# Kernel optimization log

Measured on AMD Instinct MI355X. Metric: run time of the kernel, lower is better.

## Reference

```python
import jax, jax.numpy as jnp
import numpy as np


def _prelu(x, p):
    # PReLU with a single learnable slope (torch default num_parameters=1)
    return jnp.where(x >= 0, x, p[0] * x)


def setup_inputs() -> dict:
    key = jax.random.key(0)
    ks = jax.random.split(key, 8)
    B, R, N, S, Din, Dout = 8, 4, 2048, 6, 32, 32
    return {
        "theta_param": jax.random.uniform(ks[0], (R, S), dtype=jnp.float32),
        "t_param": jax.random.uniform(ks[1], (R, S), dtype=jnp.float32),
        "a_input_batched": jax.random.uniform(ks[2], (B, R, N, N), dtype=jnp.float32),
        "x_input_batched": jax.random.normal(ks[3], (B, R, N, Din), dtype=jnp.float32),
        "fc_w": jax.random.normal(ks[4], (R, Din, Dout), dtype=jnp.float32) * 0.05,
        "fc_b": jax.random.normal(ks[5], (R, Dout), dtype=jnp.float32) * 0.05,
        "conv_w": jax.random.normal(ks[6], (R, R), dtype=jnp.float32) * 0.05,
        "conv_b": jax.random.normal(ks[7], (R,), dtype=jnp.float32) * 0.05,
        "prelu0": jnp.full((1,), 0.25, dtype=jnp.float32),
        "prelu1": jnp.full((1,), 0.25, dtype=jnp.float32),
    }


def reference(theta_param, t_param, a_input_batched, x_input_batched,
              fc_w, fc_b, conv_w, conv_b, prelu0, prelu1):
    # The inner diffusion-step loop is sum_s theta[r,s]*t[r,s] -> scalar per relation.
    coef = jnp.sum(theta_param * t_param, axis=1)              # [R]
    # diffusion_mat = coef[r] * A[b,r]; fold the scalar into the matmul result.
    diff_feat = jnp.einsum('brnm,brmd->brnd', a_input_batched, x_input_batched)
    diff_feat = coef[None, :, None, None] * diff_feat          # [B,R,N,Din]
    # Per-relation linear layer.
    fc_out = jnp.einsum('brnd,rde->brne', diff_feat, fc_w) + fc_b[None, :, None, :]
    h = _prelu(fc_out, prelu0)                                 # activation0
    # 1x1 Conv2d over the relation channel == [R,R] mixing matrix + bias.
    mixed = jnp.einsum('brne,qr->bqne', h, conv_w) + conv_b[None, :, None, None]
    latent = _prelu(mixed, prelu1)                             # activation1
    return latent  # original returns (latent, latent) — same tensor twice
```

## Files before the change

kernel.cpp:

```cpp
#include <hip/hip_runtime.h>
#include <hip/hip_bf16.h>

typedef __attribute__((ext_vector_type(8))) short  bf16x8;
typedef __attribute__((ext_vector_type(4))) float  f32x4;
typedef __attribute__((ext_vector_type(4))) int    i32x4;

#define B_   8
#define R_   4
#define N_   2048
#define S_   6
#define DIN  32
#define DOUT 32

__global__ __launch_bounds__(256) void prep_xw(
    const float* __restrict__ theta, const float* __restrict__ tpar,
    const float* __restrict__ X,     const float* __restrict__ fcw,
    __hip_bfloat16* __restrict__ xwt)
{
    int br    = blockIdx.x >> 5;
    int mtile = blockIdx.x & 31;
    int r     = br & 3;
    int t     = threadIdx.x;
    int m     = mtile * 64 + (t & 63);
    int egrp  = t >> 6;

    float coef = 0.f;
#pragma unroll
    for (int s = 0; s < S_; ++s) coef += theta[r * S_ + s] * tpar[r * S_ + s];

    const float* xrow = X + ((size_t)br * N_ + m) * DIN;
    float xr[DIN];
#pragma unroll
    for (int i = 0; i < DIN / 4; ++i) {
        f32x4 v = *(const f32x4*)(xrow + i * 4);
        xr[i * 4 + 0] = v.x; xr[i * 4 + 1] = v.y;
        xr[i * 4 + 2] = v.z; xr[i * 4 + 3] = v.w;
    }
#pragma unroll
    for (int eb = 0; eb < 8; ++eb) {
        int e = egrp * 8 + eb;
        float acc = 0.f;
#pragma unroll
        for (int d = 0; d < DIN; ++d) acc += xr[d] * fcw[(r * DIN + d) * DOUT + e];
        xwt[((size_t)br * DOUT + e) * N_ + m] = __float2bfloat16(coef * acc);
    }
}

__global__ __launch_bounds__(256) void fused_main(
    const float* __restrict__ A,   const __hip_bfloat16* __restrict__ xwt,
    const float* __restrict__ fcb, const float* __restrict__ cw,
    const float* __restrict__ cb,  const float* __restrict__ p0p,
    const float* __restrict__ p1p, float* __restrict__ out)
{
    __shared__ float hlds[R_][16][DOUT + 1];

    int b    = blockIdx.x >> 7;
    int tile = blockIdx.x & 127;
    int n0   = tile * 16;
    int t    = threadIdx.x;
    int r    = t >> 6;
    int l    = t & 63;
    int row16 = l & 15;
    int kg    = l >> 4;

    const float*  Ap  = A + (((size_t)(b * R_ + r)) * N_ + (n0 + row16)) * N_ + kg * 8;
    const ushort* xw  = (const ushort*)xwt + ((size_t)(b * R_ + r) * DOUT) * N_;
    const ushort* xw0 = xw + (size_t)row16 * N_        + kg * 8;
    const ushort* xw1 = xw + (size_t)(16 + row16) * N_ + kg * 8;

    f32x4 acc0 = {0.f, 0.f, 0.f, 0.f};
    f32x4 acc1 = {0.f, 0.f, 0.f, 0.f};

#pragma unroll 4
    for (int kt = 0; kt < N_ / 32; ++kt) {
        f32x4 a0 = *(const f32x4*)(Ap + kt * 32);
        f32x4 a1 = *(const f32x4*)(Ap + kt * 32 + 4);
        i32x4 bv0 = *(const i32x4*)(xw0 + kt * 32);
        i32x4 bv1 = *(const i32x4*)(xw1 + kt * 32);
        i32x4 av;
        asm("v_cvt_pk_bf16_f32 %0, %1, %2" : "=v"(av.x) : "v"(a0.x), "v"(a0.y));
        asm("v_cvt_pk_bf16_f32 %0, %1, %2" : "=v"(av.y) : "v"(a0.z), "v"(a0.w));
        asm("v_cvt_pk_bf16_f32 %0, %1, %2" : "=v"(av.z) : "v"(a1.x), "v"(a1.y));
        asm("v_cvt_pk_bf16_f32 %0, %1, %2" : "=v"(av.w) : "v"(a1.z), "v"(a1.w));
        bf16x8 af = __builtin_bit_cast(bf16x8, av);
        bf16x8 b0 = __builtin_bit_cast(bf16x8, bv0);
        bf16x8 b1 = __builtin_bit_cast(bf16x8, bv1);
        acc0 = __builtin_amdgcn_mfma_f32_16x16x32_bf16(af, b0, acc0, 0, 0, 0);
        acc1 = __builtin_amdgcn_mfma_f32_16x16x32_bf16(af, b1, acc1, 0, 0, 0);
    }

    float p0 = p0p[0], p1 = p1p[0];

#pragma unroll
    for (int j = 0; j < 4; ++j) {
        int rw = kg * 4 + j;
        float v0 = acc0[j] + fcb[r * DOUT + row16];
        float v1 = acc1[j] + fcb[r * DOUT + 16 + row16];
        hlds[r][rw][row16]      = v0 >= 0.f ? v0 : p0 * v0;
        hlds[r][rw][16 + row16] = v1 >= 0.f ? v1 : p0 * v1;
    }
    __syncthreads();

    int q = r;
    float c0 = cw[q * R_ + 0], c1 = cw[q * R_ + 1];
    float c2 = cw[q * R_ + 2], c3 = cw[q * R_ + 3];
    float cbq = cb[q];
    int e  = l & 31;
    int rg = l >> 5;
#pragma unroll
    for (int i = 0; i < 8; ++i) {
        int row = rg * 8 + i;
        float mx = cbq + c0 * hlds[0][row][e] + c1 * hlds[1][row][e]
                       + c2 * hlds[2][row][e] + c3 * hlds[3][row][e];
        float lat = mx >= 0.f ? mx : p1 * mx;
        out[(((size_t)b * R_ + q) * N_ + (n0 + row)) * DOUT + e] = lat;
    }
}

extern "C" void kernel_launch(void* const* d_in, const int* in_sizes, int n_in,
                              void* d_out, int out_size, void* d_ws, size_t ws_size,
                              hipStream_t stream)
{
    const float* theta = (const float*)d_in[0];
    const float* tpar  = (const float*)d_in[1];
    const float* A     = (const float*)d_in[2];
    const float* X     = (const float*)d_in[3];
    const float* fcw   = (const float*)d_in[4];
    const float* fcb   = (const float*)d_in[5];
    const float* cw    = (const float*)d_in[6];
    const float* cb    = (const float*)d_in[7];
    const float* p0    = (const float*)d_in[8];
    const float* p1    = (const float*)d_in[9];

    __hip_bfloat16* xwt = (__hip_bfloat16*)d_ws;

    prep_xw<<<B_ * R_ * (N_ / 64), 256, 0, stream>>>(theta, tpar, X, fcw, xwt);
    fused_main<<<B_ * (N_ / 16), 256, 0, stream>>>(A, xwt, fcb, cw, cb, p0, p1,
                                                   (float*)d_out);
}
```

Baseline: 154.9 us.

## Double-buffer A tiles in LDS via async global_load_lds with swizzled layout

Replaces the direct per-thread global loads of the fp32 adjacency rows with asynchronous global-to-LDS copies into a double-buffered, XOR-swizzled shared tile. Each iteration now covers 64 columns (two MFMAs per accumulator), and B operands are prefetched one step ahead with explicit vmcnt waits. The goal is to overlap the dominant A streaming with compute and hide memory latency. It adds 32KB of LDS per block, which may reduce occupancy, and relies on hand-placed waitcnts without workgroup barriers between waves, which works only because each wave owns its own LDS region.

Result: faster. 140.6 us (-9.2%).

```diff
diff --git a/kernel.cpp b/kernel.cpp
--- a/kernel.cpp
+++ b/kernel.cpp
@@ -4,6 +4,8 @@
 typedef __attribute__((ext_vector_type(8))) short  bf16x8;
 typedef __attribute__((ext_vector_type(4))) float  f32x4;
 typedef __attribute__((ext_vector_type(4))) int    i32x4;
+typedef __attribute__((address_space(3))) void       as3void;
+typedef const __attribute__((address_space(1))) void as1void;
 
 #define B_   8
 #define R_   4
@@ -11,6 +13,7 @@
 #define S_   6
 #define DIN  32
 #define DOUT 32
+#define NT   32
 
 __global__ __launch_bounds__(256) void prep_xw(
     const float* __restrict__ theta, const float* __restrict__ tpar,
@@ -52,7 +55,7 @@
     const float* __restrict__ cb,  const float* __restrict__ p0p,
     const float* __restrict__ p1p, float* __restrict__ out)
 {
-    __shared__ float hlds[R_][16][DOUT + 1];
+    __shared__ char smem[32768];
 
     int b    = blockIdx.x >> 7;
     int tile = blockIdx.x & 127;
@@ -62,35 +65,94 @@
     int l    = t & 63;
     int row16 = l & 15;
     int kg    = l >> 4;
-
-    const float*  Ap  = A + (((size_t)(b * R_ + r)) * N_ + (n0 + row16)) * N_ + kg * 8;
-    const ushort* xw  = (const ushort*)xwt + ((size_t)(b * R_ + r) * DOUT) * N_;
-    const ushort* xw0 = xw + (size_t)row16 * N_        + kg * 8;
-    const ushort* xw1 = xw + (size_t)(16 + row16) * N_ + kg * 8;
+    int swzr  = (row16 & 7) << 4;
+    int ldsbase = r * 4096;
+
+    const char* Ab = (const char*)(A + (((size_t)(b * R_ + r)) * N_ + n0) * N_);
+    const char* srcp[4];
+#pragma unroll
+    for (int i = 0; i < 4; ++i) {
+        int row = i * 4 + kg;
+        srcp[i] = Ab + (size_t)row * (N_ * 4) + (((l & 15) * 16) ^ ((row & 7) << 4));
+    }
+
+    const ushort* xw = (const ushort*)xwt + (size_t)(b * R_ + r) * DOUT * N_;
+    const ushort* bp[4];
+#pragma unroll
+    for (int eh = 0; eh < 2; ++eh)
+#pragma unroll
+        for (int m = 0; m < 2; ++m)
+            bp[eh * 2 + m] = xw + (size_t)(eh * 16 + row16) * N_ + m * 32 + kg * 8;
+
+#define STAGE_A(CUR, KT) do {                                                   \
+    _Pragma("unroll")                                                           \
+    for (int i_ = 0; i_ < 4; ++i_) {                                            \
+        __builtin_amdgcn_global_load_lds(                                       \
+            (as1void*)(srcp[i_] + (KT) * 256),                                  \
+            (as3void*)&smem[(CUR) * 16384 + ldsbase + i_ * 1024], 16, 0, 0);    \
+    } } while (0)
+
+#define LOADB(D0, D1, D2, D3, KT) do {                                          \
+    asm volatile("global_load_dwordx4 %0, %1, off" : "=v"(D0) : "v"(bp[0] + (KT) * 64)); \
+    asm volatile("global_load_dwordx4 %0, %1, off" : "=v"(D1) : "v"(bp[1] + (KT) * 64)); \
+    asm volatile("global_load_dwordx4 %0, %1, off" : "=v"(D2) : "v"(bp[2] + (KT) * 64)); \
+    asm volatile("global_load_dwordx4 %0, %1, off" : "=v"(D3) : "v"(bp[3] + (KT) * 64)); \
+    } while (0)
 
     f32x4 acc0 = {0.f, 0.f, 0.f, 0.f};
     f32x4 acc1 = {0.f, 0.f, 0.f, 0.f};
-
-#pragma unroll 4
-    for (int kt = 0; kt < N_ / 32; ++kt) {
-        f32x4 a0 = *(const f32x4*)(Ap + kt * 32);
-        f32x4 a1 = *(const f32x4*)(Ap + kt * 32 + 4);
-        i32x4 bv0 = *(const i32x4*)(xw0 + kt * 32);
-        i32x4 bv1 = *(const i32x4*)(xw1 + kt * 32);
-        i32x4 av;
-        asm("v_cvt_pk_bf16_f32 %0, %1, %2" : "=v"(av.x) : "v"(a0.x), "v"(a0.y));
-        asm("v_cvt_pk_bf16_f32 %0, %1, %2" : "=v"(av.y) : "v"(a0.z), "v"(a0.w));
-        asm("v_cvt_pk_bf16_f32 %0, %1, %2" : "=v"(av.z) : "v"(a1.x), "v"(a1.y));
-        asm("v_cvt_pk_bf16_f32 %0, %1, %2" : "=v"(av.w) : "v"(a1.z), "v"(a1.w));
-        bf16x8 af = __builtin_bit_cast(bf16x8, av);
-        bf16x8 b0 = __builtin_bit_cast(bf16x8, bv0);
-        bf16x8 b1 = __builtin_bit_cast(bf16x8, bv1);
-        acc0 = __builtin_amdgcn_mfma_f32_16x16x32_bf16(af, b0, acc0, 0, 0, 0);
-        acc1 = __builtin_amdgcn_mfma_f32_16x16x32_bf16(af, b1, acc1, 0, 0, 0);
-    }
+    i32x4 bc0, bc1, bc2, bc3, bn0, bn1, bn2, bn3;
+
+    STAGE_A(0, 0);
+    LOADB(bc0, bc1, bc2, bc3, 0);
+
+#pragma unroll 2
+    for (int kt = 0; kt < NT; ++kt) {
+        int cur = kt & 1;
+        __builtin_amdgcn_sched_barrier(0);
+        if (kt < NT - 1) {
+            STAGE_A(cur ^ 1, kt + 1);
+            LOADB(bn0, bn1, bn2, bn3, kt + 1);
+            __builtin_amdgcn_sched_barrier(0);
+            asm volatile("s_waitcnt vmcnt(8)" ::: "memory");
+        } else {
+            __builtin_amdgcn_sched_barrier(0);
+            asm volatile("s_waitcnt vmcnt(0)" ::: "memory");
+        }
+        __builtin_amdgcn_sched_barrier(0);
+
+        {
+            const char* abuf = &smem[cur * 16384 + ldsbase];
+            int base = row16 * 256 + kg * 32;
+            f32x4 lo0 = *(const f32x4*)(abuf + ((base +   0 +  0) ^ swzr));
+            f32x4 hi0 = *(const f32x4*)(abuf + ((base +   0 + 16) ^ swzr));
+            f32x4 lo1 = *(const f32x4*)(abuf + ((base + 128 +  0) ^ swzr));
+            f32x4 hi1 = *(const f32x4*)(abuf + ((base + 128 + 16) ^ swzr));
+            i32x4 av0, av1;
+            asm("v_cvt_pk_bf16_f32 %0, %1, %2" : "=v"(av0.x) : "v"(lo0.x), "v"(lo0.y));
+            asm("v_cvt_pk_bf16_f32 %0, %1, %2" : "=v"(av0.y) : "v"(lo0.z), "v"(lo0.w));
+            asm("v_cvt_pk_bf16_f32 %0, %1, %2" : "=v"(av0.z) : "v"(hi0.x), "v"(hi0.y));
+            asm("v_cvt_pk_bf16_f32 %0, %1, %2" : "=v"(av0.w) : "v"(hi0.z), "v"(hi0.w));
+            asm("v_cvt_pk_bf16_f32 %0, %1, %2" : "=v"(av1.x) : "v"(lo1.x), "v"(lo1.y));
+            asm("v_cvt_pk_bf16_f32 %0, %1, %2" : "=v"(av1.y) : "v"(lo1.z), "v"(lo1.w));
+            asm("v_cvt_pk_bf16_f32 %0, %1, %2" : "=v"(av1.z) : "v"(hi1.x), "v"(hi1.y));
+            asm("v_cvt_pk_bf16_f32 %0, %1, %2" : "=v"(av1.w) : "v"(hi1.z), "v"(hi1.w));
+            bf16x8 a0 = __builtin_bit_cast(bf16x8, av0);
+            bf16x8 a1 = __builtin_bit_cast(bf16x8, av1);
+            acc0 = __builtin_amdgcn_mfma_f32_16x16x32_bf16(a0, __builtin_bit_cast(bf16x8, bc0), acc0, 0, 0, 0);
+            acc0 = __builtin_amdgcn_mfma_f32_16x16x32_bf16(a1, __builtin_bit_cast(bf16x8, bc1), acc0, 0, 0, 0);
+            acc1 = __builtin_amdgcn_mfma_f32_16x16x32_bf16(a0, __builtin_bit_cast(bf16x8, bc2), acc1, 0, 0, 0);
+            acc1 = __builtin_amdgcn_mfma_f32_16x16x32_bf16(a1, __builtin_bit_cast(bf16x8, bc3), acc1, 0, 0, 0);
+        }
+        bc0 = bn0; bc1 = bn1; bc2 = bn2; bc3 = bn3;
+    }
+#undef STAGE_A
+#undef LOADB
 
     float p0 = p0p[0], p1 = p1p[0];
 
+    __syncthreads();
+    float (*hlds)[16][DOUT + 1] = (float (*)[16][DOUT + 1])(void*)smem;
 #pragma unroll
     for (int j = 0; j < 4; ++j) {
         int rw = kg * 4 + j;
```

## Double-buffer A tiles in LDS via direct global-to-LDS loads with software prefetch

Applied to the files above, without the earlier changes.

The main GEMM loop now streams the fp32 adjacency tiles into a swizzled, double-buffered LDS region using global_load_lds, 128 columns per stage. The matching bf16 B fragments are prefetched one stage ahead into registers with inline-asm loads and explicit vmcnt waits. The aim is to keep more memory requests in flight and hide latency on this bandwidth-bound read of A, which is the dominant traffic. In exchange the kernel uses a 64 KB static LDS buffer, which limits blocks per CU, and it depends on hand-managed waitcnt and sched_barrier ordering.

New measurement: 138.6 us. 1.12x faster.

```diff
diff --git a/kernel.cpp b/kernel.cpp
--- a/kernel.cpp
+++ b/kernel.cpp
@@ -4,6 +4,8 @@
 typedef __attribute__((ext_vector_type(8))) short  bf16x8;
 typedef __attribute__((ext_vector_type(4))) float  f32x4;
 typedef __attribute__((ext_vector_type(4))) int    i32x4;
+typedef __attribute__((address_space(3))) void       as3void;
+typedef const __attribute__((address_space(1))) void as1void;
 
 #define B_   8
 #define R_   4
@@ -11,6 +13,7 @@
 #define S_   6
 #define DIN  32
 #define DOUT 32
+#define NT   16
 
 __global__ __launch_bounds__(256) void prep_xw(
     const float* __restrict__ theta, const float* __restrict__ tpar,
@@ -52,7 +55,7 @@
     const float* __restrict__ cb,  const float* __restrict__ p0p,
     const float* __restrict__ p1p, float* __restrict__ out)
 {
-    __shared__ float hlds[R_][16][DOUT + 1];
+    __shared__ char smem[65536];
 
     int b    = blockIdx.x >> 7;
     int tile = blockIdx.x & 127;
@@ -62,35 +65,96 @@
     int l    = t & 63;
     int row16 = l & 15;
     int kg    = l >> 4;
-
-    const float*  Ap  = A + (((size_t)(b * R_ + r)) * N_ + (n0 + row16)) * N_ + kg * 8;
-    const ushort* xw  = (const ushort*)xwt + ((size_t)(b * R_ + r) * DOUT) * N_;
-    const ushort* xw0 = xw + (size_t)row16 * N_        + kg * 8;
-    const ushort* xw1 = xw + (size_t)(16 + row16) * N_ + kg * 8;
+    int swzr  = (row16 & 7) << 4;
+    int ldsbase = r * 8192;
+    int hl   = l >> 5;
+    int l31  = l & 31;
+
+    const char* Ab = (const char*)(A + (((size_t)(b * R_ + r)) * N_ + n0) * N_);
+    const char* srcp[8];
+#pragma unroll
+    for (int i = 0; i < 8; ++i) {
+        int row = 2 * i + hl;
+        srcp[i] = Ab + (size_t)row * (N_ * 4) + ((l31 * 16) ^ ((row & 7) << 4));
+    }
+
+    const ushort* xw  = (const ushort*)xwt + (size_t)(b * R_ + r) * DOUT * N_;
+    const ushort* bp0 = xw + (size_t)row16 * N_        + kg * 8;
+    const ushort* bp1 = xw + (size_t)(16 + row16) * N_ + kg * 8;
+
+#define STAGE_A(CUR, KT) do {                                                    \
+    _Pragma("unroll")                                                            \
+    for (int i_ = 0; i_ < 8; ++i_) {                                             \
+        __builtin_amdgcn_global_load_lds(                                        \
+            (as1void*)(srcp[i_] + (size_t)(KT) * 512),                           \
+            (as3void*)&smem[(CUR) * 32768 + ldsbase + i_ * 1024], 16, 0, 0);     \
+    } } while (0)
+
+#define LOADB(P, KT) do {                                                        \
+    asm volatile("global_load_dwordx4 %0, %1, off" : "=v"(P##0) : "v"(bp0 + (KT) * 128 +  0)); \
+    asm volatile("global_load_dwordx4 %0, %1, off" : "=v"(P##1) : "v"(bp0 + (KT) * 128 + 32)); \
+    asm volatile("global_load_dwordx4 %0, %1, off" : "=v"(P##2) : "v"(bp0 + (KT) * 128 + 64)); \
+    asm volatile("global_load_dwordx4 %0, %1, off" : "=v"(P##3) : "v"(bp0 + (KT) * 128 + 96)); \
+    asm volatile("global_load_dwordx4 %0, %1, off" : "=v"(P##4) : "v"(bp1 + (KT) * 128 +  0)); \
+    asm volatile("global_load_dwordx4 %0, %1, off" : "=v"(P##5) : "v"(bp1 + (KT) * 128 + 32)); \
+    asm volatile("global_load_dwordx4 %0, %1, off" : "=v"(P##6) : "v"(bp1 + (KT) * 128 + 64)); \
+    asm volatile("global_load_dwordx4 %0, %1, off" : "=v"(P##7) : "v"(bp1 + (KT) * 128 + 96)); \
+    } while (0)
 
     f32x4 acc0 = {0.f, 0.f, 0.f, 0.f};
     f32x4 acc1 = {0.f, 0.f, 0.f, 0.f};
-
-#pragma unroll 4
-    for (int kt = 0; kt < N_ / 32; ++kt) {
-        f32x4 a0 = *(const f32x4*)(Ap + kt * 32);
-        f32x4 a1 = *(const f32x4*)(Ap + kt * 32 + 4);
-        i32x4 bv0 = *(const i32x4*)(xw0 + kt * 32);
-        i32x4 bv1 = *(const i32x4*)(xw1 + kt * 32);
-        i32x4 av;
-        asm("v_cvt_pk_bf16_f32 %0, %1, %2" : "=v"(av.x) : "v"(a0.x), "v"(a0.y));
-        asm("v_cvt_pk_bf16_f32 %0, %1, %2" : "=v"(av.y) : "v"(a0.z), "v"(a0.w));
-        asm("v_cvt_pk_bf16_f32 %0, %1, %2" : "=v"(av.z) : "v"(a1.x), "v"(a1.y));
-        asm("v_cvt_pk_bf16_f32 %0, %1, %2" : "=v"(av.w) : "v"(a1.z), "v"(a1.w));
-        bf16x8 af = __builtin_bit_cast(bf16x8, av);
-        bf16x8 b0 = __builtin_bit_cast(bf16x8, bv0);
-        bf16x8 b1 = __builtin_bit_cast(bf16x8, bv1);
-        acc0 = __builtin_amdgcn_mfma_f32_16x16x32_bf16(af, b0, acc0, 0, 0, 0);
-        acc1 = __builtin_amdgcn_mfma_f32_16x16x32_bf16(af, b1, acc1, 0, 0, 0);
-    }
+    i32x4 bc0, bc1, bc2, bc3, bc4, bc5, bc6, bc7;
+    i32x4 bn0, bn1, bn2, bn3, bn4, bn5, bn6, bn7;
+
+    STAGE_A(0, 0);
+    LOADB(bc, 0);
+
+#pragma unroll 2
+    for (int kt = 0; kt < NT; ++kt) {
+        int cur = kt & 1;
+        __builtin_amdgcn_sched_barrier(0);
+        if (kt < NT - 1) {
+            STAGE_A(cur ^ 1, kt + 1);
+            LOADB(bn, kt + 1);
+            __builtin_amdgcn_sched_barrier(0);
+            asm volatile("s_waitcnt vmcnt(16)" ::: "memory");
+        } else {
+            __builtin_amdgcn_sched_barrier(0);
+            asm volatile("s_waitcnt vmcnt(0)" ::: "memory");
+        }
+        __builtin_amdgcn_sched_barrier(0);
+
+        {
+            const char* abuf = &smem[cur * 32768 + ldsbase];
+            int rbase = row16 * 512;
+#define KSTEP(KS, BA, BB) do {                                                   \
+    f32x4 lo = *(const f32x4*)(abuf + rbase + (((KS) * 128 + kg * 32 +  0) ^ swzr)); \
+    f32x4 hi = *(const f32x4*)(abuf + rbase + (((KS) * 128 + kg * 32 + 16) ^ swzr)); \
+    i32x4 av;                                                                    \
+    asm("v_cvt_pk_bf16_f32 %0, %1, %2" : "=v"(av.x) : "v"(lo.x), "v"(lo.y));     \
+    asm("v_cvt_pk_bf16_f32 %0, %1, %2" : "=v"(av.y) : "v"(lo.z), "v"(lo.w));     \
+    asm("v_cvt_pk_bf16_f32 %0, %1, %2" : "=v"(av.z) : "v"(hi.x), "v"(hi.y));     \
+    asm("v_cvt_pk_bf16_f32 %0, %1, %2" : "=v"(av.w) : "v"(hi.z), "v"(hi.w));     \
+    bf16x8 af = __builtin_bit_cast(bf16x8, av);                                  \
+    acc0 = __builtin_amdgcn_mfma_f32_16x16x32_bf16(af, __builtin_bit_cast(bf16x8, BA), acc0, 0, 0, 0); \
+    acc1 = __builtin_amdgcn_mfma_f32_16x16x32_bf16(af, __builtin_bit_cast(bf16x8, BB), acc1, 0, 0, 0); \
+    } while (0)
+            KSTEP(0, bc0, bc4);
+            KSTEP(1, bc1, bc5);
+            KSTEP(2, bc2, bc6);
+            KSTEP(3, bc3, bc7);
+#undef KSTEP
+        }
+        bc0 = bn0; bc1 = bn1; bc2 = bn2; bc3 = bn3;
+        bc4 = bn4; bc5 = bn5; bc6 = bn6; bc7 = bn7;
+    }
+#undef STAGE_A
+#undef LOADB
 
     float p0 = p0p[0], p1 = p1p[0];
 
+    __syncthreads();
+    float (*hlds)[16][DOUT + 1] = (float (*)[16][DOUT + 1])(void*)smem;
 #pragma unroll
     for (int j = 0; j < 4; ++j) {
         int rw = kg * 4 + j;
```
